# Kernel tuning notes

Measured on AMD Instinct MI355X. Metric: run time of the kernel, lower is better.

Reference implementation:

```python
import jax, jax.numpy as jnp
import numpy as np

M1 = M2 = 16      # spectral modes
CM1 = CM2 = 4     # cft modes = modes // 4
L_SEG = 4
M_CHEB = 8
PAD = 9


def _cft2d(x):
    # x: [B,C,H,W]; H,W divisible by L_SEG, segment length divisible by M_CHEB
    B, C, H, W = x.shape
    hs, ws = H // L_SEG, W // L_SEG
    seg = x.reshape(B, C, L_SEG, hs, L_SEG, ws).transpose(0, 1, 2, 4, 3, 5)
    seg = seg.reshape(B, C, L_SEG * L_SEG, hs * ws)  # row-major segment order (i,j)
    seg = seg / jnp.maximum(jnp.linalg.norm(seg, axis=-1, keepdims=True), 1e-12)
    # torch x[:,:,k::M].mean over k=0..M-1 == reshape (n//M, M), mean over rows
    coeffs = seg.reshape(B, C, L_SEG * L_SEG, (hs * ws) // M_CHEB, M_CHEB).mean(axis=3)
    coeffs = coeffs.reshape(B, C, -1)[:, :, : CM1 * CM2]
    return coeffs.reshape(B, C, CM1, CM2)  # real part; imag part is zero


def _spectral_rc(x, w1, w2, g1w, g1b, g2w, g2b):
    B, C, H, W = x.shape
    xft = jnp.fft.rfft2(x, axes=(-2, -1))
    top = jnp.einsum('bixy,ioxy->boxy', xft[:, :, :M1, :M2], w1)
    bot = jnp.einsum('bixy,ioxy->boxy', xft[:, :, H - M1:, :M2], w2)
    out_ft = jnp.zeros((B, w1.shape[1], H, W // 2 + 1), dtype=xft.dtype)
    out_ft = out_ft.at[:, :, :M1, :M2].set(top)
    out_ft = out_ft.at[:, :, H - M1:, :M2].set(bot)
    x_fno = jnp.fft.irfft2(out_ft, s=(H, W), axes=(-2, -1))
    cr = _cft2d(x)
    # torch.view_as_real interleaves (real, imag) on last axis; imag == 0
    cflat = jnp.stack([cr, jnp.zeros_like(cr)], axis=-1).reshape(B, -1)
    h = jax.nn.gelu(cflat @ g1w.T + g1b, approximate=False)
    corr = h @ g2w.T + g2b  # [B, C_out]
    return x_fno + corr[:, :, None, None]


def _forward(x, sw1r, sw1i, sw2r, sw2i, g1w, g1b, g2w, g2b, cw, cb,
             fc0w, fc0b, fc1w, fc1b, fc2w, fc2b):
    B, S1, S2, _ = x.shape
    gx = jnp.broadcast_to(jnp.linspace(0., 1., S1, dtype=x.dtype)[None, :, None, None], (B, S1, S2, 1))
    gy = jnp.broadcast_to(jnp.linspace(0., 1., S2, dtype=x.dtype)[None, None, :, None], (B, S1, S2, 1))
    h = jnp.concatenate([x, gx, gy], axis=-1) @ fc0w.T + fc0b
    h = h.transpose(0, 3, 1, 2)
    h = jnp.pad(h, ((0, 0), (0, 0), (0, PAD), (0, PAD)))
    for l in range(4):
        w1 = sw1r[l] + 1j * sw1i[l]
        w2 = sw2r[l] + 1j * sw2i[l]
        h1 = _spectral_rc(h, w1, w2, g1w[l], g1b[l], g2w[l], g2b[l])
        h2 = jnp.einsum('bchw,oc->bohw', h, cw[l]) + cb[l][None, :, None, None]
        h = h1 + h2
        if l < 3:
            h = jax.nn.gelu(h, approximate=False)
    h = h[..., :-PAD, :-PAD].transpose(0, 2, 3, 1)
    h = jax.nn.gelu(h @ fc1w.T + fc1b, approximate=False)
    return h @ fc2w.T + fc2b


def setup_inputs():
    key = jax.random.key(0)
    ks = jax.random.split(key, 20)
    B, S, Cin, Cout, Wd = 8, 119, 3, 1, 64
    f32 = jnp.float32
    scale = 1.0 / (Wd * Wd)
    return {
        'x': jax.random.normal(ks[0], (B, S, S, Cin), f32),
        'sw1r': scale * jax.random.uniform(ks[1], (4, Wd, Wd, M1, M2), f32),
        'sw1i': scale * jax.random.uniform(ks[2], (4, Wd, Wd, M1, M2), f32),
        'sw2r': scale * jax.random.uniform(ks[3], (4, Wd, Wd, M1, M2), f32),
        'sw2i': scale * jax.random.uniform(ks[4], (4, Wd, Wd, M1, M2), f32),
        'g1w': 0.02 * jax.random.normal(ks[5], (4, 256, 2048), f32),
        'g1b': 0.02 * jax.random.normal(ks[6], (4, 256), f32),
        'g2w': 0.02 * jax.random.normal(ks[7], (4, Wd, 256), f32),
        'g2b': 0.02 * jax.random.normal(ks[8], (4, Wd), f32),
        'cw': (1.0 / 8.0) * jax.random.normal(ks[9], (4, Wd, Wd), f32),
        'cb': 0.1 * jax.random.normal(ks[10], (4, Wd), f32),
        'fc0w': 0.4 * jax.random.normal(ks[11], (Wd, Cin + 2), f32),
        'fc0b': 0.1 * jax.random.normal(ks[12], (Wd,), f32),
        'fc1w': (1.0 / 8.0) * jax.random.normal(ks[13], (128, Wd), f32),
        'fc1b': 0.1 * jax.random.normal(ks[14], (128,), f32),
        'fc2w': (1.0 / 11.3) * jax.random.normal(ks[15], (Cout, 128), f32),
        'fc2b': 0.1 * jax.random.normal(ks[16], (Cout,), f32),
    }


def reference(x, sw1r, sw1i, sw2r, sw2i, g1w, g1b, g2w, g2b, cw, cb,
              fc0w, fc0b, fc1w, fc1b, fc2w, fc2b):
    return _forward(x, sw1r, sw1i, sw2r, sw2i, g1w, g1b, g2w, g2b, cw, cb,
                    fc0w, fc0b, fc1w, fc1b, fc2w, fc2b)
```

## Files before the change

kernel.cpp:

```cpp
#include <hip/hip_runtime.h>
#include <math.h>

#define NB 8
#define NC 64
#define NH 128
#define NW 128
#define NS 119
#define NPIX 113288

__device__ __forceinline__ float gelu_f(float v) {
    return 0.5f * v * (1.0f + erff(v * 0.70710678118654752f));
}

__global__ void __launch_bounds__(128) k_trig(float2* __restrict__ trig) {
    int t = threadIdx.x;
    double a = (double)t * (3.14159265358979323846 / 64.0);
    trig[t] = make_float2((float)cos(a), (float)sin(a));
}

__global__ void __launch_bounds__(128) k_tab(float2* __restrict__ wd) {
    int idx = blockIdx.x * 128 + threadIdx.x;
    int ky = idx >> 7, w = idx & 127;
    int prod = (ky * w) & 127;
    double a = (double)prod * (3.14159265358979323846 / 64.0);
    wd[idx] = make_float2((float)cos(a), (float)(-sin(a)));
}

__global__ void __launch_bounds__(256) k_tc(const float* __restrict__ fc1w,
                                            const float* __restrict__ cw,
                                            float* __restrict__ fc1wT,
                                            float* __restrict__ cwT) {
    int u = blockIdx.x * 256 + threadIdx.x;
    if (u < 8192) {
        int c = u >> 7, j = u & 127;
        fc1wT[u] = fc1w[j * 64 + c];
    } else {
        int v = u - 8192;
        int l = v >> 12, idx = v & 4095;
        int c = idx >> 6, o = idx & 63;
        cwT[v] = cw[l * 4096 + o * 64 + c];
    }
}

__global__ void __launch_bounds__(256) k_fc0(const float* __restrict__ x,
                                             const float* __restrict__ w,
                                             const float* __restrict__ bia,
                                             float* __restrict__ h) {
    __shared__ float sw[320];
    __shared__ float sb[64];
    int t = threadIdx.x;
    for (int u = t; u < 320; u += 256) sw[u] = w[u];
    if (t < 64) sb[t] = bia[t];
    __syncthreads();
    int p = blockIdx.x * 256 + t;
    int b = p >> 14;
    int rem = p & 16383;
    int r = rem >> 7, wc = rem & 127;
    float v0 = 0.f, v1 = 0.f, v2 = 0.f, gx = 0.f, gy = 0.f;
    bool inside = (r < NS) && (wc < NS);
    if (inside) {
        const float* xp = x + ((size_t)(b * NS + r) * NS + wc) * 3;
        v0 = xp[0]; v1 = xp[1]; v2 = xp[2];
        gx = (float)r * (1.0f / 118.0f);
        gy = (float)wc * (1.0f / 118.0f);
    }
    float* hp = h + (size_t)b * NC * NH * NW + rem;
    for (int c = 0; c < 64; ++c) {
        float val = 0.f;
        if (inside) {
            const float* wr = sw + c * 5;
            val = v0 * wr[0] + v1 * wr[1] + v2 * wr[2] + gx * wr[3] + gy * wr[4] + sb[c];
        }
        hp[c * (NH * NW)] = val;
    }
}

__global__ void __launch_bounds__(256) k_mlp1(const float* __restrict__ cr,
                                              const float* __restrict__ g1w,
                                              const float* __restrict__ g1b,
                                              float* __restrict__ hmid) {
    __shared__ float s_cr[8][1024];
    __shared__ float s_wave[4][8];
    int j = blockIdx.x;
    int t = threadIdx.x;
    {
        float* sp = &s_cr[0][0];
        for (int u = t; u < 8192; u += 256) sp[u] = cr[u];
    }
    const float* wrow = g1w + (size_t)j * 2048;
    int v0 = t * 4;
    float w0 = wrow[2 * v0], w1 = wrow[2 * v0 + 2], w2 = wrow[2 * v0 + 4], w3 = wrow[2 * v0 + 6];
    __syncthreads();
    float acc[8];
#pragma unroll
    for (int b = 0; b < 8; ++b) {
        const float* cp = s_cr[b] + v0;
        acc[b] = cp[0] * w0 + cp[1] * w1 + cp[2] * w2 + cp[3] * w3;
    }
#pragma unroll
    for (int d = 32; d > 0; d >>= 1) {
#pragma unroll
        for (int b = 0; b < 8; ++b) acc[b] += __shfl_down(acc[b], d, 64);
    }
    int wv = t >> 6;
    if ((t & 63) == 0) {
#pragma unroll
        for (int b = 0; b < 8; ++b) s_wave[wv][b] = acc[b];
    }
    __syncthreads();
    if (t < 8) {
        float a = s_wave[0][t] + s_wave[1][t] + s_wave[2][t] + s_wave[3][t] + g1b[j];
        hmid[t * 256 + j] = gelu_f(a);
    }
}

__global__ void __launch_bounds__(256) k_mlp2(const float* __restrict__ hmid,
                                              const float* __restrict__ g2w,
                                              const float* __restrict__ g2b,
                                              float* __restrict__ corr) {
    __shared__ float s_h[2048];
    __shared__ float s_w[256];
    int o = blockIdx.x;
    int t = threadIdx.x;
    s_w[t] = g2w[o * 256 + t];
    for (int u = t; u < 2048; u += 256) s_h[u] = hmid[u];
    __syncthreads();
    int b = t >> 5, k = t & 31;
    const float* hp = s_h + b * 256 + k * 8;
    const float* wp = s_w + k * 8;
    float acc = 0.f;
#pragma unroll
    for (int i = 0; i < 8; ++i) acc += hp[i] * wp[i];
#pragma unroll
    for (int d = 16; d > 0; d >>= 1) acc += __shfl_down(acc, d, 32);
    if (k == 0) corr[b * 64 + o] = acc + g2b[o];
}

__global__ void __launch_bounds__(256) k_dft2(const float* __restrict__ h,
                                              float2* __restrict__ xft,
                                              float* __restrict__ cr,
                                              const float2* __restrict__ wd,
                                              const float2* __restrict__ trig) {
    __shared__ __align__(16) float sx[16][132];
    __shared__ __align__(16) float2 sW[16][134];
    __shared__ float2 sT[128][17];
    __shared__ float2 st[128];
    __shared__ float s_cs[2][16][8];
    __shared__ float s_cq[2][16][8];
    int t = threadIdx.x;
    int bc = blockIdx.x;
    if (t < 128) st[t] = trig[t];
    for (int u = t; u < 2048; u += 256) sW[u >> 7][u & 127] = wd[u];
    const float* src = h + (size_t)bc * 16384;
    int r = t >> 4, ky = t & 15;
    float c0a = 0.f, c1a = 0.f, q0a = 0.f, q1a = 0.f;
    for (int ch = 0; ch < 8; ++ch) {
        __syncthreads();
        for (int u = t; u < 2048; u += 256) sx[u >> 7][u & 127] = src[ch * 2048 + u];
        __syncthreads();
        const float* xr = sx[r];
        const float2* wk = sW[ky];
        float re = 0.f, im = 0.f;
#pragma unroll 8
        for (int w0 = 0; w0 < 128; w0 += 4) {
            float4 x4 = *(const float4*)(xr + w0);
            float4 w01 = *(const float4*)(wk + w0);
            float4 w23 = *(const float4*)(wk + w0 + 2);
            re += x4.x * w01.x; im += x4.x * w01.y;
            re += x4.y * w01.z; im += x4.y * w01.w;
            re += x4.z * w23.x; im += x4.z * w23.y;
            re += x4.w * w23.z; im += x4.w * w23.w;
        }
        sT[ch * 16 + r][ky] = make_float2(re, im);
        if (ch < 2 && t < 128) {
            int rr = t >> 3, k = t & 7;
            const float* row = sx[rr];
#pragma unroll
            for (int g = 0; g < 4; ++g) {
                float a = row[g * 8 + k];       c0a += a;  q0a += a * a;
                float bv = row[32 + g * 8 + k]; c1a += bv; q1a += bv * bv;
            }
            if (ch == 1) {
                s_cs[0][rr][k] = c0a; s_cs[1][rr][k] = c1a;
                s_cq[0][rr][k] = q0a; s_cq[1][rr][k] = q1a;
            }
        }
    }
    __syncthreads();
    int mlo = t >> 4;
    int kxa = mlo, kxb = 112 + mlo;
    float2 sva = st[kxa]; float sca = sva.x, ssa = -sva.y;
    float2 svb = st[kxb]; float scb = svb.x, ssb = -svb.y;
    float rea = 0.f, ima = 0.f, reb = 0.f, imb = 0.f;
    for (int h0 = 0; h0 < 128; h0 += 16) {
        float2 bva = st[(kxa * h0) & 127]; float cca = bva.x, csa = -bva.y;
        float2 bvb = st[(kxb * h0) & 127]; float ccb = bvb.x, csb = -bvb.y;
#pragma unroll
        for (int j = 0; j < 16; ++j) {
            float2 Tv = sT[h0 + j][ky];
            rea += Tv.x * cca - Tv.y * csa;
            ima += Tv.x * csa + Tv.y * cca;
            reb += Tv.x * ccb - Tv.y * csb;
            imb += Tv.x * csb + Tv.y * ccb;
            float na = cca * sca - csa * ssa; csa = cca * ssa + csa * sca; cca = na;
            float nb = ccb * scb - csb * ssb; csb = ccb * ssb + csb * scb; ccb = nb;
        }
    }
    float2* xp = xft + (size_t)bc * 512;
    xp[mlo * 16 + ky] = make_float2(rea, ima);
    xp[(mlo + 16) * 16 + ky] = make_float2(reb, imb);
    if (t < 16) {
        int half = t >> 3, k = t & 7;
        float s = 0.f, q = 0.f;
#pragma unroll
        for (int rr = 0; rr < 16; ++rr) s += s_cs[half][rr][k];
        for (int rr = 0; rr < 16; ++rr)
#pragma unroll
            for (int kk = 0; kk < 8; ++kk) q += s_cq[half][rr][kk];
        float norm = fmaxf(sqrtf(q), 1e-12f);
        cr[bc * 16 + t] = s / (128.0f * norm);
    }
}

__global__ void __launch_bounds__(512) k_mix(const float2* __restrict__ xft,
                                             const float* __restrict__ w1r,
                                             const float* __restrict__ w1i,
                                             const float* __restrict__ w2r,
                                             const float* __restrict__ w2i,
                                             float2* __restrict__ F) {
    int rbid = blockIdx.x;
    int m = (rbid & 7) + 8 * ((rbid >> 3) & 3);
    int e = rbid >> 5;
    __shared__ float2 s_w[64][64];
    __shared__ float2 s_x[8][64];
    int t = threadIdx.x;
    const float* wr; const float* wi; int mm;
    if (m < 16) { wr = w1r; wi = w1i; mm = m; } else { wr = w2r; wi = w2i; mm = m - 16; }
    int off = mm * 16 + e;
    for (int u = t; u < 4096; u += 512) {
        s_w[u >> 6][u & 63] = make_float2(wr[(u << 8) + off], wi[(u << 8) + off]);
    }
    {
        int bb = t >> 6, i = t & 63;
        s_x[bb][i] = xft[((size_t)(bb * 64 + i) * 32 + m) * 16 + e];
    }
    __syncthreads();
    int bb = t >> 6, o = t & 63;
    float re = 0.f, im = 0.f;
#pragma unroll 8
    for (int i = 0; i < 64; ++i) {
        float2 xv = s_x[bb][i];
        float2 wv = s_w[i][o];
        re += xv.x * wv.x - xv.y * wv.y;
        im += xv.x * wv.y + xv.y * wv.x;
    }
    F[((size_t)(bb * 16 + e) * 32 + m) * 64 + o] = make_float2(re, im);
}

__global__ void __launch_bounds__(256) k_inva(const float2* __restrict__ F,
                                              float2* __restrict__ G,
                                              const float2* __restrict__ trig) {
    int blk = blockIdx.x;
    int hh = blk & 7;
    int ky = (blk >> 3) & 15;
    int b  = blk >> 7;
    __shared__ float2 s_f[32][64];
    __shared__ float2 s_t[128];
    int t = threadIdx.x;
    if (t < 128) s_t[t] = trig[t];
    for (int u = t; u < 2048; u += 256)
        s_f[u >> 6][u & 63] = F[(size_t)(b * 16 + ky) * 2048 + u];
    __syncthreads();
    int o = t & 63, hq = t >> 6;
    int h0 = hh * 16 + hq * 4;
    float accr[4], acci[4];
#pragma unroll
    for (int u = 0; u < 4; ++u) { accr[u] = 0.f; acci[u] = 0.f; }
    for (int m = 0; m < 32; ++m) {
        int kx = (m < 16) ? m : (96 + m);
        float2 f  = s_f[m][o];
        float2 stp = s_t[kx];
        float2 c0  = s_t[(kx * h0) & 127];
        float zr = f.x * c0.x - f.y * c0.y;
        float zi = f.x * c0.y + f.y * c0.x;
#pragma unroll
        for (int u = 0; u < 4; ++u) {
            accr[u] += zr; acci[u] += zi;
            float nz = zr * stp.x - zi * stp.y;
            zi = zr * stp.y + zi * stp.x;
            zr = nz;
        }
    }
    size_t gbase = ((size_t)(b * 128 + h0) * 16 + ky) * 64 + o;
#pragma unroll
    for (int u = 0; u < 4; ++u)
        G[gbase + (size_t)u * 1024] = make_float2(accr[u], acci[u]);
}

__global__ void __launch_bounds__(256, 4) k_invb(const float2* __restrict__ G,
                                                 const float* __restrict__ hin,
                                                 const float* __restrict__ cwTl,
                                                 const float* __restrict__ cbl,
                                                 const float* __restrict__ corr,
                                                 const float2* __restrict__ trig,
                                                 float* __restrict__ hout,
                                                 int do_gelu) {
    int blk = blockIdx.x;
    int b = blk >> 7, h = blk & 127;
    __shared__ __align__(16) float s_cwT[64][64];
    __shared__ __align__(16) float2 s_g[16][64];
    __shared__ __align__(16) float s_h[16][128];
    __shared__ float2 s_t[128];
    __shared__ float s_co[64];
    int t = threadIdx.x;
    if (t < 128) s_t[t] = trig[t];
    if (t < 64) s_co[t] = corr[b * 64 + t] + cbl[t];
    {
        float* cw0 = &s_cwT[0][0];
        for (int u = t; u < 4096; u += 256) cw0[u] = cwTl[u];
    }
    {
        const float2* gp = G + (size_t)(b * 128 + h) * 1024;
        for (int u = t; u < 1024; u += 256) s_g[u >> 6][u & 63] = gp[u];
    }
    __syncthreads();
    int ot2 = t >> 6;
    int wt6 = t & 63;
    int o0 = ot2 * 16;
    float acc[16][2];
#pragma unroll
    for (int i = 0; i < 16; ++i) { acc[i][0] = 0.f; acc[i][1] = 0.f; }
    float2 rw0 = s_t[wt6];
    float2 rw1 = s_t[wt6 + 64];
    float z0r = 1.f, z0i = 0.f, z1r = 1.f, z1i = 0.f;
    for (int ky = 0; ky < 16; ++ky) {
        float fs = (ky == 0) ? 1.f : 2.f;
        float tc0 = fs * z0r, ts0 = fs * z0i;
        float tc1 = fs * z1r, ts1 = fs * z1i;
        const float4* gk = (const float4*)(&s_g[ky][o0]);
#pragma unroll
        for (int i2 = 0; i2 < 8; ++i2) {
            float4 g2 = gk[i2];
            acc[2*i2][0]   += g2.x * tc0 - g2.y * ts0;
            acc[2*i2][1]   += g2.x * tc1 - g2.y * ts1;
            acc[2*i2+1][0] += g2.z * tc0 - g2.w * ts0;
            acc[2*i2+1][1] += g2.z * tc1 - g2.w * ts1;
        }
        float nz0 = z0r * rw0.x - z0i * rw0.y; z0i = z0r * rw0.y + z0i * rw0.x; z0r = nz0;
        float nz1 = z1r * rw1.x - z1i * rw1.y; z1i = z1r * rw1.y + z1i * rw1.x; z1r = nz1;
    }
    const float invn = 1.0f / 16384.0f;
#pragma unroll
    for (int i = 0; i < 16; ++i) { acc[i][0] *= invn; acc[i][1] *= invn; }
    for (int cc = 0; cc < 64; cc += 16) {
        __syncthreads();
        for (int u = t; u < 2048; u += 256) {
            int c = u >> 7, w = u & 127;
            s_h[c][w] = hin[((size_t)(b * 64 + cc + c) * 128 + h) * 128 + w];
        }
        __syncthreads();
        for (int c = 0; c < 16; ++c) {
            float hv0 = s_h[c][wt6];
            float hv1 = s_h[c][wt6 + 64];
            const float4* cwp = (const float4*)(&s_cwT[cc + c][o0]);
#pragma unroll
            for (int i4 = 0; i4 < 4; ++i4) {
                float4 cv = cwp[i4];
                acc[4*i4][0]   += cv.x * hv0; acc[4*i4][1]   += cv.x * hv1;
                acc[4*i4+1][0] += cv.y * hv0; acc[4*i4+1][1] += cv.y * hv1;
                acc[4*i4+2][0] += cv.z * hv0; acc[4*i4+2][1] += cv.z * hv1;
                acc[4*i4+3][0] += cv.w * hv0; acc[4*i4+3][1] += cv.w * hv1;
            }
        }
    }
#pragma unroll
    for (int i = 0; i < 16; ++i) {
        int o = o0 + i;
        float co = s_co[o];
        float* outp = hout + ((size_t)(b * 64 + o) * 128 + h) * 128;
        float v0 = acc[i][0] + co;
        float v1 = acc[i][1] + co;
        if (do_gelu) { v0 = gelu_f(v0); v1 = gelu_f(v1); }
        outp[wt6] = v0;
        outp[wt6 + 64] = v1;
    }
}

__global__ void __launch_bounds__(256, 2) k_invbh(const float2* __restrict__ G,
                                                  const float* __restrict__ hin,
                                                  const float* __restrict__ cwTl,
                                                  const float* __restrict__ cbl,
                                                  const float* __restrict__ corr,
                                                  const float2* __restrict__ trig,
                                                  const float* __restrict__ fc1wT,
                                                  const float* __restrict__ fc1b,
                                                  const float* __restrict__ fc2w,
                                                  const float* __restrict__ fc2b,
                                                  float* __restrict__ out) {
    int blk = blockIdx.x;
    int b = blk / 119;
    int h = blk - b * 119;
    __shared__ __align__(16) char smem[32768];
    float*  s_cwT = (float*)smem;
    float2* s_g   = (float2*)(smem + 16384);
    float*  s_hh  = (float*)(smem + 24576);
    float*  s_hall= (float*)smem;
    __shared__ __align__(16) float s_w8[16][128];
    __shared__ float2 s_t[128];
    __shared__ float s_co[64];
    __shared__ float s_b1[128];
    __shared__ float s_w2[128];
    __shared__ float s_red[4][132];
    int t = threadIdx.x;
    if (t < 128) s_t[t] = trig[t];
    else { s_b1[t - 128] = fc1b[t - 128]; s_w2[t - 128] = fc2w[t - 128]; }
    if (t < 64) s_co[t] = corr[b * 64 + t] + cbl[t];
    for (int u = t; u < 4096; u += 256) s_cwT[u] = cwTl[u];
    {
        const float2* gp = G + (size_t)(b * 128 + h) * 1024;
        for (int u = t; u < 1024; u += 256) s_g[u] = gp[u];
    }
    __syncthreads();
    int ot2 = t >> 6;
    int wt6 = t & 63;
    int o0 = ot2 * 16;
    float acc[16][2];
#pragma unroll
    for (int i = 0; i < 16; ++i) { acc[i][0] = 0.f; acc[i][1] = 0.f; }
    float2 rw0 = s_t[wt6];
    float2 rw1 = s_t[wt6 + 64];
    float z0r = 1.f, z0i = 0.f, z1r = 1.f, z1i = 0.f;
    for (int ky = 0; ky < 16; ++ky) {
        float fs = (ky == 0) ? 1.f : 2.f;
        float tc0 = fs * z0r, ts0 = fs * z0i;
        float tc1 = fs * z1r, ts1 = fs * z1i;
        const float4* gk = (const float4*)(s_g + ky * 64 + o0);
#pragma unroll
        for (int i2 = 0; i2 < 8; ++i2) {
            float4 g2 = gk[i2];
            acc[2*i2][0]   += g2.x * tc0 - g2.y * ts0;
            acc[2*i2][1]   += g2.x * tc1 - g2.y * ts1;
            acc[2*i2+1][0] += g2.z * tc0 - g2.w * ts0;
            acc[2*i2+1][1] += g2.z * tc1 - g2.w * ts1;
        }
        float nz0 = z0r * rw0.x - z0i * rw0.y; z0i = z0r * rw0.y + z0i * rw0.x; z0r = nz0;
        float nz1 = z1r * rw1.x - z1i * rw1.y; z1i = z1r * rw1.y + z1i * rw1.x; z1r = nz1;
    }
    const float invn = 1.0f / 16384.0f;
#pragma unroll
    for (int i = 0; i < 16; ++i) { acc[i][0] *= invn; acc[i][1] *= invn; }
    for (int cc = 0; cc < 64; cc += 16) {
        __syncthreads();
        for (int u = t; u < 2048; u += 256) {
            int c = u >> 7, w = u & 127;
            s_hh[c * 128 + w] = hin[((size_t)(b * 64 + cc + c) * 128 + h) * 128 + w];
        }
        __syncthreads();
        for (int c = 0; c < 16; ++c) {
            float hv0 = s_hh[c * 128 + wt6];
            float hv1 = s_hh[c * 128 + wt6 + 64];
            const float4* cwp = (const float4*)(s_cwT + (cc + c) * 64 + o0);
#pragma unroll
            for (int i4 = 0; i4 < 4; ++i4) {
                float4 cv = cwp[i4];
                acc[4*i4][0]   += cv.x * hv0; acc[4*i4][1]   += cv.x * hv1;
                acc[4*i4+1][0] += cv.y * hv0; acc[4*i4+1][1] += cv.y * hv1;
                acc[4*i4+2][0] += cv.z * hv0; acc[4*i4+2][1] += cv.z * hv1;
                acc[4*i4+3][0] += cv.w * hv0; acc[4*i4+3][1] += cv.w * hv1;
            }
        }
    }
    __syncthreads();
#pragma unroll
    for (int i = 0; i < 16; ++i) {
        float co = s_co[o0 + i];
        s_hall[(o0 + i) * 128 + wt6]      = acc[i][0] + co;
        s_hall[(o0 + i) * 128 + wt6 + 64] = acc[i][1] + co;
    }
    int j0 = ot2 * 32;
    float a32[32][2];
#pragma unroll
    for (int i = 0; i < 32; ++i) { a32[i][0] = 0.f; a32[i][1] = 0.f; }
    for (int cc = 0; cc < 64; cc += 16) {
        __syncthreads();
        for (int u = t; u < 2048; u += 256)
            s_w8[u >> 7][u & 127] = fc1wT[(cc + (u >> 7)) * 128 + (u & 127)];
        __syncthreads();
        for (int c = 0; c < 16; ++c) {
            float hv0 = s_hall[(cc + c) * 128 + wt6];
            float hv1 = s_hall[(cc + c) * 128 + wt6 + 64];
            const float4* wp = (const float4*)(&s_w8[c][j0]);
#pragma unroll
            for (int q = 0; q < 8; ++q) {
                float4 wx = wp[q];
                a32[4*q][0]   += wx.x * hv0; a32[4*q][1]   += wx.x * hv1;
                a32[4*q+1][0] += wx.y * hv0; a32[4*q+1][1] += wx.y * hv1;
                a32[4*q+2][0] += wx.z * hv0; a32[4*q+2][1] += wx.z * hv1;
                a32[4*q+3][0] += wx.w * hv0; a32[4*q+3][1] += wx.w * hv1;
            }
        }
    }
    float sum0 = 0.f, sum1 = 0.f;
#pragma unroll
    for (int i = 0; i < 32; ++i) {
        float b1 = s_b1[j0 + i];
        float w2 = s_w2[j0 + i];
        sum0 += gelu_f(a32[i][0] + b1) * w2;
        sum1 += gelu_f(a32[i][1] + b1) * w2;
    }
    s_red[ot2][wt6] = sum0;
    s_red[ot2][wt6 + 64] = sum1;
    __syncthreads();
    if (t < NS) {
        out[b * (NS * NS) + h * NS + t] =
            fc2b[0] + s_red[0][t] + s_red[1][t] + s_red[2][t] + s_red[3][t];
    }
}

extern "C" void kernel_launch(void* const* d_in, const int* in_sizes, int n_in,
                              void* d_out, int out_size, void* d_ws, size_t ws_size,
                              hipStream_t stream) {
    const float* x    = (const float*)d_in[0];
    const float* sw1r = (const float*)d_in[1];
    const float* sw1i = (const float*)d_in[2];
    const float* sw2r = (const float*)d_in[3];
    const float* sw2i = (const float*)d_in[4];
    const float* g1w  = (const float*)d_in[5];
    const float* g1b  = (const float*)d_in[6];
    const float* g2w  = (const float*)d_in[7];
    const float* g2b  = (const float*)d_in[8];
    const float* cw   = (const float*)d_in[9];
    const float* cb   = (const float*)d_in[10];
    const float* fc0w = (const float*)d_in[11];
    const float* fc0b = (const float*)d_in[12];
    const float* fc1w = (const float*)d_in[13];
    const float* fc1b = (const float*)d_in[14];
    const float* fc2w = (const float*)d_in[15];
    const float* fc2b = (const float*)d_in[16];
    float* out = (float*)d_out;

    char* ws = (char*)d_ws;
    const size_t SZ_H   = (size_t)NB * NC * NH * NW * 4;
    const size_t SZ_XFT = (size_t)NB * NC * 32 * 16 * 8;
    const size_t SZ_F   = SZ_XFT;
    const size_t SZ_G   = (size_t)NB * NH * 16 * 64 * 8;
    size_t off = 0;
    float2* trig = (float2*)(ws + off); off += 1024;
    float2* wdft = (float2*)(ws + off); off += 2048 * 8;
    float*  f1T  = (float*)(ws + off);  off += 8192 * 4;
    float*  cwT  = (float*)(ws + off);  off += 16384 * 4;
    float*  hA   = (float*)(ws + off);  off += SZ_H;
    float*  hB   = (float*)(ws + off);  off += SZ_H;
    float2* xft  = (float2*)(ws + off); off += SZ_XFT;
    float2* F    = (float2*)(ws + off); off += SZ_F;
    float2* G    = (float2*)(ws + off); off += SZ_G;
    float*  cr   = (float*)(ws + off);  off += (size_t)NB * NC * 16 * 4;
    float*  hmid = (float*)(ws + off);  off += (size_t)NB * 256 * 4;
    float*  corr = (float*)(ws + off);  off += (size_t)NB * 64 * 4;
    (void)ws_size; (void)in_sizes; (void)n_in; (void)out_size;

    k_trig<<<1, 128, 0, stream>>>(trig);
    k_tab<<<16, 128, 0, stream>>>(wdft);
    k_tc<<<96, 256, 0, stream>>>(fc1w, cw, f1T, cwT);
    k_fc0<<<512, 256, 0, stream>>>(x, fc0w, fc0b, hA);

    float* hcur = hA;
    float* hnxt = hB;
    for (int l = 0; l < 4; ++l) {
        const float* w1r = sw1r + (size_t)l * 1048576;
        const float* w1i = sw1i + (size_t)l * 1048576;
        const float* w2r = sw2r + (size_t)l * 1048576;
        const float* w2i = sw2i + (size_t)l * 1048576;
        const float* g1w_l = g1w + (size_t)l * 524288;
        const float* g1b_l = g1b + l * 256;
        const float* g2w_l = g2w + (size_t)l * 16384;
        const float* g2b_l = g2b + l * 64;
        const float* cwT_l = cwT + (size_t)l * 4096;
        const float* cb_l  = cb + l * 64;

        k_dft2<<<512, 256, 0, stream>>>(hcur, xft, cr, wdft, trig);
        k_mlp1<<<256, 256, 0, stream>>>(cr, g1w_l, g1b_l, hmid);
        k_mlp2<<<64, 256, 0, stream>>>(hmid, g2w_l, g2b_l, corr);
        k_mix<<<512, 512, 0, stream>>>(xft, w1r, w1i, w2r, w2i, F);
        k_inva<<<1024, 256, 0, stream>>>(F, G, trig);
        if (l < 3) {
            k_invb<<<1024, 256, 0, stream>>>(G, hcur, cwT_l, cb_l, corr, trig, hnxt, 1);
            float* tmp = hcur; hcur = hnxt; hnxt = tmp;
        } else {
            k_invbh<<<NB * NS, 256, 0, stream>>>(G, hcur, cwT_l, cb_l, corr, trig,
                                                 f1T, fc1b, fc2w, fc2b, out);
        }
    }
}
```

Baseline: 544.7 us.

## Fuse inverse H-direction DFT into final inverse kernels and read h directly

Removes the separate k_inva kernel and its intermediate G buffer: each k_invb/k_invbh block now computes its own row's 16x64 partial inverse DFT over the 32 kx modes directly from F, using a twiddle recurrence. The 1x1-conv input h is also read straight from global memory into registers rather than staged through shared memory with barriers. This removes one launch per layer and the G write/read round trip, but each block redundantly reads all of F for its batch (32 KB per block) and performs more arithmetic, and the register-held h loads are strided per channel.

```diff
diff --git a/kernel.cpp b/kernel.cpp
--- a/kernel.cpp
+++ b/kernel.cpp
@@ -257,47 +257,7 @@
     F[((size_t)(bb * 16 + e) * 32 + m) * 64 + o] = make_float2(re, im);
 }
 
-__global__ void __launch_bounds__(256) k_inva(const float2* __restrict__ F,
-                                              float2* __restrict__ G,
-                                              const float2* __restrict__ trig) {
-    int blk = blockIdx.x;
-    int hh = blk & 7;
-    int ky = (blk >> 3) & 15;
-    int b  = blk >> 7;
-    __shared__ float2 s_f[32][64];
-    __shared__ float2 s_t[128];
-    int t = threadIdx.x;
-    if (t < 128) s_t[t] = trig[t];
-    for (int u = t; u < 2048; u += 256)
-        s_f[u >> 6][u & 63] = F[(size_t)(b * 16 + ky) * 2048 + u];
-    __syncthreads();
-    int o = t & 63, hq = t >> 6;
-    int h0 = hh * 16 + hq * 4;
-    float accr[4], acci[4];
-#pragma unroll
-    for (int u = 0; u < 4; ++u) { accr[u] = 0.f; acci[u] = 0.f; }
-    for (int m = 0; m < 32; ++m) {
-        int kx = (m < 16) ? m : (96 + m);
-        float2 f  = s_f[m][o];
-        float2 stp = s_t[kx];
-        float2 c0  = s_t[(kx * h0) & 127];
-        float zr = f.x * c0.x - f.y * c0.y;
-        float zi = f.x * c0.y + f.y * c0.x;
-#pragma unroll
-        for (int u = 0; u < 4; ++u) {
-            accr[u] += zr; acci[u] += zi;
-            float nz = zr * stp.x - zi * stp.y;
-            zi = zr * stp.y + zi * stp.x;
-            zr = nz;
-        }
-    }
-    size_t gbase = ((size_t)(b * 128 + h0) * 16 + ky) * 64 + o;
-#pragma unroll
-    for (int u = 0; u < 4; ++u)
-        G[gbase + (size_t)u * 1024] = make_float2(accr[u], acci[u]);
-}
-
-__global__ void __launch_bounds__(256, 4) k_invb(const float2* __restrict__ G,
+__global__ void __launch_bounds__(256, 4) k_invb(const float2* __restrict__ F,
                                                  const float* __restrict__ hin,
                                                  const float* __restrict__ cwTl,
                                                  const float* __restrict__ cbl,
@@ -309,7 +269,6 @@
     int b = blk >> 7, h = blk & 127;
     __shared__ __align__(16) float s_cwT[64][64];
     __shared__ __align__(16) float2 s_g[16][64];
-    __shared__ __align__(16) float s_h[16][128];
     __shared__ float2 s_t[128];
     __shared__ float s_co[64];
     int t = threadIdx.x;
@@ -320,8 +279,40 @@
         for (int u = t; u < 4096; u += 256) cw0[u] = cwTl[u];
     }
     {
-        const float2* gp = G + (size_t)(b * 128 + h) * 1024;
-        for (int u = t; u < 1024; u += 256) s_g[u >> 6][u & 63] = gp[u];
+        float2 rot = trig[h];
+        int o = t & 63, ky0 = t >> 6;
+        const float2* Fb = F + (size_t)b * 32768 + o;
+        float a0r=0.f,a0i=0.f,a1r=0.f,a1i=0.f,a2r=0.f,a2i=0.f,a3r=0.f,a3i=0.f;
+        float zr = 1.f, zi = 0.f;
+        for (int m = 0; m < 16; ++m) {
+            const float2* fm = Fb + m * 64;
+            float2 f0 = fm[(ky0     ) * 2048];
+            float2 f1 = fm[(ky0 +  4) * 2048];
+            float2 f2 = fm[(ky0 +  8) * 2048];
+            float2 f3 = fm[(ky0 + 12) * 2048];
+            a0r += f0.x*zr - f0.y*zi; a0i += f0.x*zi + f0.y*zr;
+            a1r += f1.x*zr - f1.y*zi; a1i += f1.x*zi + f1.y*zr;
+            a2r += f2.x*zr - f2.y*zi; a2i += f2.x*zi + f2.y*zr;
+            a3r += f3.x*zr - f3.y*zi; a3i += f3.x*zi + f3.y*zr;
+            float nz = zr*rot.x - zi*rot.y; zi = zr*rot.y + zi*rot.x; zr = nz;
+        }
+        float z2r = zr, z2i = -zi;
+        for (int m = 16; m < 32; ++m) {
+            const float2* fm = Fb + m * 64;
+            float2 f0 = fm[(ky0     ) * 2048];
+            float2 f1 = fm[(ky0 +  4) * 2048];
+            float2 f2 = fm[(ky0 +  8) * 2048];
+            float2 f3 = fm[(ky0 + 12) * 2048];
+            a0r += f0.x*z2r - f0.y*z2i; a0i += f0.x*z2i + f0.y*z2r;
+            a1r += f1.x*z2r - f1.y*z2i; a1i += f1.x*z2i + f1.y*z2r;
+            a2r += f2.x*z2r - f2.y*z2i; a2i += f2.x*z2i + f2.y*z2r;
+            a3r += f3.x*z2r - f3.y*z2i; a3i += f3.x*z2i + f3.y*z2r;
+            float nz = z2r*rot.x - z2i*rot.y; z2i = z2r*rot.y + z2i*rot.x; z2r = nz;
+        }
+        s_g[ky0     ][o] = make_float2(a0r, a0i);
+        s_g[ky0 +  4][o] = make_float2(a1r, a1i);
+        s_g[ky0 +  8][o] = make_float2(a2r, a2i);
+        s_g[ky0 + 12][o] = make_float2(a3r, a3i);
     }
     __syncthreads();
     int ot2 = t >> 6;
@@ -352,24 +343,24 @@
     const float invn = 1.0f / 16384.0f;
 #pragma unroll
     for (int i = 0; i < 16; ++i) { acc[i][0] *= invn; acc[i][1] *= invn; }
-    for (int cc = 0; cc < 64; cc += 16) {
-        __syncthreads();
-        for (int u = t; u < 2048; u += 256) {
-            int c = u >> 7, w = u & 127;
-            s_h[c][w] = hin[((size_t)(b * 64 + cc + c) * 128 + h) * 128 + w];
-        }
-        __syncthreads();
-        for (int c = 0; c < 16; ++c) {
-            float hv0 = s_h[c][wt6];
-            float hv1 = s_h[c][wt6 + 64];
+    const float* hp = hin + ((size_t)(b * 64) * 128 + h) * 128;
+    for (int cc = 0; cc < 64; cc += 4) {
+        float hv0[4], hv1[4];
+#pragma unroll
+        for (int c = 0; c < 4; ++c) {
+            hv0[c] = hp[(size_t)(cc + c) * 16384 + wt6];
+            hv1[c] = hp[(size_t)(cc + c) * 16384 + wt6 + 64];
+        }
+#pragma unroll
+        for (int c = 0; c < 4; ++c) {
             const float4* cwp = (const float4*)(&s_cwT[cc + c][o0]);
 #pragma unroll
             for (int i4 = 0; i4 < 4; ++i4) {
                 float4 cv = cwp[i4];
-                acc[4*i4][0]   += cv.x * hv0; acc[4*i4][1]   += cv.x * hv1;
-                acc[4*i4+1][0] += cv.y * hv0; acc[4*i4+1][1] += cv.y * hv1;
-                acc[4*i4+2][0] += cv.z * hv0; acc[4*i4+2][1] += cv.z * hv1;
-                acc[4*i4+3][0] += cv.w * hv0; acc[4*i4+3][1] += cv.w * hv1;
+                acc[4*i4][0]   += cv.x * hv0[c]; acc[4*i4][1]   += cv.x * hv1[c];
+                acc[4*i4+1][0] += cv.y * hv0[c]; acc[4*i4+1][1] += cv.y * hv1[c];
+                acc[4*i4+2][0] += cv.z * hv0[c]; acc[4*i4+2][1] += cv.z * hv1[c];
+                acc[4*i4+3][0] += cv.w * hv0[c]; acc[4*i4+3][1] += cv.w * hv1[c];
             }
         }
     }
@@ -386,7 +377,7 @@
     }
 }
 
-__global__ void __launch_bounds__(256, 2) k_invbh(const float2* __restrict__ G,
+__global__ void __launch_bounds__(256, 2) k_invbh(const float2* __restrict__ F,
                                                   const float* __restrict__ hin,
                                                   const float* __restrict__ cwTl,
                                                   const float* __restrict__ cbl,
@@ -403,7 +394,6 @@
     __shared__ __align__(16) char smem[32768];
     float*  s_cwT = (float*)smem;
     float2* s_g   = (float2*)(smem + 16384);
-    float*  s_hh  = (float*)(smem + 24576);
     float*  s_hall= (float*)smem;
     __shared__ __align__(16) float s_w8[16][128];
     __shared__ float2 s_t[128];
@@ -417,8 +407,41 @@
     if (t < 64) s_co[t] = corr[b * 64 + t] + cbl[t];
     for (int u = t; u < 4096; u += 256) s_cwT[u] = cwTl[u];
     {
-        const float2* gp = G + (size_t)(b * 128 + h) * 1024;
-        for (int u = t; u < 1024; u += 256) s_g[u] = gp[u];
+        float2 rot = trig[h];
+        int o = t & 63, ky0 = t >> 6;
+        const float2* Fb = F + (size_t)b * 32768 + o;
+        float a0r=0.f,a0i=0.f,a1r=0.f,a1i=0.f,a2r=0.f,a2i=0.f,a3r=0.f,a3i=0.f;
+        float zr = 1.f, zi = 0.f;
+        for (int m = 0; m < 16; ++m) {
+            const float2* fm = Fb + m * 64;
+            float2 f0 = fm[(ky0     ) * 2048];
+            float2 f1 = fm[(ky0 +  4) * 2048];
+            float2 f2 = fm[(ky0 +  8) * 2048];
+            float2 f3 = fm[(ky0 + 12) * 2048];
+            a0r += f0.x*zr - f0.y*zi; a0i += f0.x*zi + f0.y*zr;
+            a1r += f1.x*zr - f1.y*zi; a1i += f1.x*zi + f1.y*zr;
+            a2r += f2.x*zr - f2.y*zi; a2i += f2.x*zi + f2.y*zr;
+            a3r += f3.x*zr - f3.y*zi; a3i += f3.x*zi + f3.y*zr;
+            float nz = zr*rot.x - zi*rot.y; zi = zr*rot.y + zi*rot.x; zr = nz;
+        }
+        float z2r = zr, z2i = -zi;
+        for (int m = 16; m < 32; ++m) {
+            const float2* fm = Fb + m * 64;
+            float2 f0 = fm[(ky0     ) * 2048];
+            float2 f1 = fm[(ky0 +  4) * 2048];
+            float2 f2 = fm[(ky0 +  8) * 2048];
+            float2 f3 = fm[(ky0 + 12) * 2048];
+            a0r += f0.x*z2r - f0.y*z2i; a0i += f0.x*z2i + f0.y*z2r;
+            a1r += f1.x*z2r - f1.y*z2i; a1i += f1.x*z2i + f1.y*z2r;
+            a2r += f2.x*z2r - f2.y*z2i; a2i += f2.x*z2i + f2.y*z2r;
+            a3r += f3.x*z2r - f3.y*z2i; a3i += f3.x*z2i + f3.y*z2r;
+            float nz = z2r*rot.x - z2i*rot.y; z2i = z2r*rot.y + z2i*rot.x; z2r = nz;
+        }
+        float2* sg = (float2*)(smem + 16384);
+        sg[(ky0     ) * 64 + o] = make_float2(a0r, a0i);
+        sg[(ky0 +  4) * 64 + o] = make_float2(a1r, a1i);
+        sg[(ky0 +  8) * 64 + o] = make_float2(a2r, a2i);
+        sg[(ky0 + 12) * 64 + o] = make_float2(a3r, a3i);
     }
     __syncthreads();
     int ot2 = t >> 6;
@@ -449,24 +472,24 @@
     const float invn = 1.0f / 16384.0f;
 #pragma unroll
     for (int i = 0; i < 16; ++i) { acc[i][0] *= invn; acc[i][1] *= invn; }
-    for (int cc = 0; cc < 64; cc += 16) {
-        __syncthreads();
-        for (int u = t; u < 2048; u += 256) {
-            int c = u >> 7, w = u & 127;
-            s_hh[c * 128 + w] = hin[((size_t)(b * 64 + cc + c) * 128 + h) * 128 + w];
-        }
-        __syncthreads();
-        for (int c = 0; c < 16; ++c) {
-            float hv0 = s_hh[c * 128 + wt6];
-            float hv1 = s_hh[c * 128 + wt6 + 64];
+    const float* hp = hin + ((size_t)(b * 64) * 128 + h) * 128;
+    for (int cc = 0; cc < 64; cc += 8) {
+        float hv0[8], hv1[8];
+#pragma unroll
+        for (int c = 0; c < 8; ++c) {
+            hv0[c] = hp[(size_t)(cc + c) * 16384 + wt6];
+            hv1[c] = hp[(size_t)(cc + c) * 16384 + wt6 + 64];
+        }
+#pragma unroll
+        for (int c = 0; c < 8; ++c) {
             const float4* cwp = (const float4*)(s_cwT + (cc + c) * 64 + o0);
 #pragma unroll
             for (int i4 = 0; i4 < 4; ++i4) {
                 float4 cv = cwp[i4];
-                acc[4*i4][0]   += cv.x * hv0; acc[4*i4][1]   += cv.x * hv1;
-                acc[4*i4+1][0] += cv.y * hv0; acc[4*i4+1][1] += cv.y * hv1;
-                acc[4*i4+2][0] += cv.z * hv0; acc[4*i4+2][1] += cv.z * hv1;
-                acc[4*i4+3][0] += cv.w * hv0; acc[4*i4+3][1] += cv.w * hv1;
+                acc[4*i4][0]   += cv.x * hv0[c]; acc[4*i4][1]   += cv.x * hv1[c];
+                acc[4*i4+1][0] += cv.y * hv0[c]; acc[4*i4+1][1] += cv.y * hv1[c];
+                acc[4*i4+2][0] += cv.z * hv0[c]; acc[4*i4+2][1] += cv.z * hv1[c];
+                acc[4*i4+3][0] += cv.w * hv0[c]; acc[4*i4+3][1] += cv.w * hv1[c];
             }
         }
     }
@@ -543,7 +566,6 @@
     const size_t SZ_H   = (size_t)NB * NC * NH * NW * 4;
     const size_t SZ_XFT = (size_t)NB * NC * 32 * 16 * 8;
     const size_t SZ_F   = SZ_XFT;
-    const size_t SZ_G   = (size_t)NB * NH * 16 * 64 * 8;
     size_t off = 0;
     float2* trig = (float2*)(ws + off); off += 1024;
     float2* wdft = (float2*)(ws + off); off += 2048 * 8;
@@ -553,7 +575,6 @@
     float*  hB   = (float*)(ws + off);  off += SZ_H;
     float2* xft  = (float2*)(ws + off); off += SZ_XFT;
     float2* F    = (float2*)(ws + off); off += SZ_F;
-    float2* G    = (float2*)(ws + off); off += SZ_G;
     float*  cr   = (float*)(ws + off);  off += (size_t)NB * NC * 16 * 4;
     float*  hmid = (float*)(ws + off);  off += (size_t)NB * 256 * 4;
     float*  corr = (float*)(ws + off);  off += (size_t)NB * 64 * 4;
@@ -582,12 +603,11 @@
         k_mlp1<<<256, 256, 0, stream>>>(cr, g1w_l, g1b_l, hmid);
         k_mlp2<<<64, 256, 0, stream>>>(hmid, g2w_l, g2b_l, corr);
         k_mix<<<512, 512, 0, stream>>>(xft, w1r, w1i, w2r, w2i, F);
-        k_inva<<<1024, 256, 0, stream>>>(F, G, trig);
         if (l < 3) {
-            k_invb<<<1024, 256, 0, stream>>>(G, hcur, cwT_l, cb_l, corr, trig, hnxt, 1);
+            k_invb<<<1024, 256, 0, stream>>>(F, hcur, cwT_l, cb_l, corr, trig, hnxt, 1);
             float* tmp = hcur; hcur = hnxt; hnxt = tmp;
         } else {
-            k_invbh<<<NB * NS, 256, 0, stream>>>(G, hcur, cwT_l, cb_l, corr, trig,
+            k_invbh<<<NB * NS, 256, 0, stream>>>(F, hcur, cwT_l, cb_l, corr, trig,
                                                  f1T, fc1b, fc2w, fc2b, out);
         }
     }
```

After: 510.8 us. 1.07x faster.
